# Kernel optimization log

Measured on AMD Instinct MI355X. Metric: run time of the kernel, lower is better.

## Reference

```python
import jax, jax.numpy as jnp
import numpy as np

DIST_THRESH = 150.0
ROW_EPS = 1e-6
BN_EPS = 1e-5


def setup_inputs() -> dict:
    key = jax.random.key(0)
    ks = jax.random.split(key, 6)
    B, N, T, D = 64, 64, 16, 512
    person_features = jax.random.normal(ks[0], (B, N, T, D), dtype=jnp.float32)
    # bboxes in pixel-ish units so the 150px threshold gives a mixed adjacency
    bboxes = jax.random.uniform(ks[1], (B, N, 4), dtype=jnp.float32) * 300.0
    w1 = jax.random.normal(ks[2], (D, D), dtype=jnp.float32) * (1.0 / np.sqrt(D))
    b1 = jax.random.normal(ks[3], (D,), dtype=jnp.float32) * 0.02
    w2 = jax.random.normal(ks[4], (D, D), dtype=jnp.float32) * (1.0 / np.sqrt(D))
    b2 = jax.random.normal(ks[5], (D,), dtype=jnp.float32) * 0.02
    g1 = jnp.ones((D,), jnp.float32); beta1 = jnp.zeros((D,), jnp.float32)
    g2 = jnp.ones((D,), jnp.float32); beta2 = jnp.zeros((D,), jnp.float32)
    return {"person_features": person_features, "bboxes": bboxes,
            "w1": w1, "b1": b1, "g1": g1, "beta1": beta1,
            "w2": w2, "b2": b2, "g2": g2, "beta2": beta2}


def _build_adjacency(bboxes):
    # centers: (B, N, 2) from x+w/2, y+h/2
    cx = bboxes[..., 0] + 0.5 * bboxes[..., 2]
    cy = bboxes[..., 1] + 0.5 * bboxes[..., 3]
    centers = jnp.stack([cx, cy], axis=-1)
    # pairwise distances (B, N, N), vectorized (replaces B*N*N python loop)
    diff = centers[:, :, None, :] - centers[:, None, :, :]
    dist = jnp.sqrt(jnp.sum(diff * diff, axis=-1))
    N = bboxes.shape[1]
    eye = jnp.eye(N, dtype=bboxes.dtype)
    off_diag = (eye[None] == 0.0)
    A = jnp.where((dist < DIST_THRESH) & off_diag, 1.0, 0.0) + eye[None]
    return A


def _stgcn(x, A, w, b, g, beta):
    # x: (B, N, C); A: (B, N, N)
    # torch: A_norm = A / (A.sum(dim=1 of A[i] -> axis=2) + eps)
    A_norm = A / (jnp.sum(A, axis=2, keepdims=True) + ROW_EPS)
    # x_graph = x[b].T @ A_norm[b]  -> (B, C, N)
    y = jnp.einsum('bnc,bnm->bcm', x, A_norm)
    # 1x1 conv == channel GEMM, bias added per out-channel
    y = jnp.einsum('oc,bcm->bom', w, y) + b[None, :, None]
    # BatchNorm2d in training mode: biased stats over (batch, spatial)
    mean = jnp.mean(y, axis=(0, 2), keepdims=True)
    var = jnp.mean(jnp.square(y - mean), axis=(0, 2), keepdims=True)
    y = (y - mean) / jnp.sqrt(var + BN_EPS)
    y = y * g[None, :, None] + beta[None, :, None]
    y = jax.nn.relu(y)
    return jnp.swapaxes(y, 1, 2)  # (B, N, C)


def reference(person_features, bboxes, w1, b1, g1, beta1, w2, b2, g2, beta2):
    A = _build_adjacency(bboxes)
    x = person_features[:, :, -1, :]  # (B, N, D) last frame
    h = _stgcn(x, A, w1, b1, g1, beta1)
    h = _stgcn(h, A, w2, b2, g2, beta2)
    # write enhanced features back into last timestep
    return person_features.at[:, :, -1, :].set(h)
```

## Files before the change

### kernel.cpp

```cpp
#include <hip/hip_runtime.h>
#include <hip/hip_bf16.h>


typedef __attribute__((ext_vector_type(8))) short short8;
typedef __attribute__((ext_vector_type(4))) float v4f;

#define DIST_THRESH 150.0f
#define ROW_EPS 1e-6f
#define BN_EPS 1e-5f

__device__ __forceinline__ ushort f2bf(float f) {
  union { __hip_bfloat16 h; ushort u; } cv;
  cv.h = __float2bfloat16(f);
  return cv.u;
}

__global__ __launch_bounds__(256) void k_copy_prep(const float4* __restrict__ in,
                                                   float4* __restrict__ out,
                                                   const float* __restrict__ w1,
                                                   const float* __restrict__ w2,
                                                   ushort* __restrict__ wb,
                                                   float* __restrict__ stats) {
  int blk = blockIdx.x;
  int t = threadIdx.x;
  if (blk < 8192) {
    size_t i = (size_t)blk * 256 + t;
#pragma unroll
    for (int j = 0; j < 4; ++j) {
      size_t idx = i + (size_t)j * 2097152;
      int tt = (int)((idx >> 7) & 15);
      if (tt != 15) out[idx] = in[idx];
    }
  } else {
    int idx = (blk - 8192) * 256 + t;
    float v = (idx < 262144) ? w1[idx] : w2[idx - 262144];
    wb[idx] = f2bf(v);
    if (idx < 2048) stats[idx] = 0.f;
  }
}

__global__ __launch_bounds__(256) void k_agg(const float* __restrict__ Xbase,
                                             int rowStride,
                                             const float* __restrict__ bb,
                                             const float* __restrict__ stats,
                                             const float* __restrict__ g,
                                             const float* __restrict__ beta,
                                             int applyBN,
                                             ushort* __restrict__ Z) {
  int b = blockIdx.x;
  int c0 = blockIdx.y * 128;
  int t = threadIdx.x;
  __shared__ float Xs[64][128];
  __shared__ float As[64][64];
  __shared__ float cxs[64], cys[64];
  __shared__ float scaleS[128], shiftS[128];

  if (t < 64) {
    float4 v = *(const float4*)&bb[(size_t)(b * 64 + t) * 4];
    cxs[t] = v.x + 0.5f * v.z;
    cys[t] = v.y + 0.5f * v.w;
  }
  if (applyBN && t < 32) {
    int c = t * 4;
    float4 sm = *(const float4*)&stats[c0 + c];
    float4 sq = *(const float4*)&stats[512 + c0 + c];
    float4 gg = *(const float4*)&g[c0 + c];
    float4 bt = *(const float4*)&beta[c0 + c];
    const float inv = 1.0f / 4096.0f;
    float mean, var, sc;
    mean = sm.x * inv; var = sq.x * inv - mean * mean; sc = gg.x * rsqrtf(var + BN_EPS);
    scaleS[c] = sc; shiftS[c] = bt.x - mean * sc;
    mean = sm.y * inv; var = sq.y * inv - mean * mean; sc = gg.y * rsqrtf(var + BN_EPS);
    scaleS[c + 1] = sc; shiftS[c + 1] = bt.y - mean * sc;
    mean = sm.z * inv; var = sq.z * inv - mean * mean; sc = gg.z * rsqrtf(var + BN_EPS);
    scaleS[c + 2] = sc; shiftS[c + 2] = bt.z - mean * sc;
    mean = sm.w * inv; var = sq.w * inv - mean * mean; sc = gg.w * rsqrtf(var + BN_EPS);
    scaleS[c + 3] = sc; shiftS[c + 3] = bt.w - mean * sc;
  }
  __syncthreads();

  if (t < 64) {
    float mycx = cxs[t], mycy = cys[t];
    float rs = 0.f;
    for (int m = 0; m < 64; ++m) {
      float dx = mycx - cxs[m], dy = mycy - cys[m];
      float d = sqrtf(dx * dx + dy * dy);
      float a = (m == t) ? 1.0f : ((d < DIST_THRESH) ? 1.0f : 0.0f);
      rs += a;
    }
    float inv = 1.0f / (rs + ROW_EPS);
    for (int m = 0; m < 64; ++m) {
      float dx = mycx - cxs[m], dy = mycy - cys[m];
      float d = sqrtf(dx * dx + dy * dy);
      float a = (m == t) ? 1.0f : ((d < DIST_THRESH) ? 1.0f : 0.0f);
      As[t][m] = a * inv;
    }
  }

  const float* xb = Xbase + (size_t)b * 64 * rowStride;
  for (int i = t; i < 2048; i += 256) {
    int n = i >> 5, c4 = (i & 31) << 2;
    float4 x = *(const float4*)&xb[(size_t)n * rowStride + c0 + c4];
    if (applyBN) {
      x.x = fmaxf(x.x * scaleS[c4] + shiftS[c4], 0.f);
      x.y = fmaxf(x.y * scaleS[c4 + 1] + shiftS[c4 + 1], 0.f);
      x.z = fmaxf(x.z * scaleS[c4 + 2] + shiftS[c4 + 2], 0.f);
      x.w = fmaxf(x.w * scaleS[c4 + 3] + shiftS[c4 + 3], 0.f);
    }
    *(float4*)&Xs[n][c4] = x;
  }
  __syncthreads();

  int c4 = (t & 31) << 2;
  int m0 = (t >> 5) << 3;
  float4 acc[8];
#pragma unroll
  for (int i = 0; i < 8; ++i) acc[i] = make_float4(0.f, 0.f, 0.f, 0.f);

  for (int n = 0; n < 64; ++n) {
    float4 x = *(const float4*)&Xs[n][c4];
    float4 a0 = *(const float4*)&As[n][m0];
    float4 a1 = *(const float4*)&As[n][m0 + 4];
    float as[8] = {a0.x, a0.y, a0.z, a0.w, a1.x, a1.y, a1.z, a1.w};
#pragma unroll
    for (int i = 0; i < 8; ++i) {
      acc[i].x = fmaf(as[i], x.x, acc[i].x);
      acc[i].y = fmaf(as[i], x.y, acc[i].y);
      acc[i].z = fmaf(as[i], x.z, acc[i].z);
      acc[i].w = fmaf(as[i], x.w, acc[i].w);
    }
  }

  size_t zbase = (size_t)b * 64 * 512 + c0 + c4;
#pragma unroll
  for (int i = 0; i < 8; ++i) {
    int m = m0 + i;
    ushort4 zz;
    zz.x = f2bf(acc[i].x);
    zz.y = f2bf(acc[i].y);
    zz.z = f2bf(acc[i].z);
    zz.w = f2bf(acc[i].w);
    *(ushort4*)&Z[zbase + (size_t)m * 512] = zz;
  }
}

__global__ __launch_bounds__(256) void k_gemm(const ushort* __restrict__ Z,
                                              const ushort* __restrict__ W,
                                              const float* __restrict__ bias,
                                              float* __restrict__ Y,
                                              float* __restrict__ sum,
                                              float* __restrict__ sumsq) {
  __shared__ __align__(16) ushort Zs[64 * 40];
  __shared__ __align__(16) ushort Ws[64 * 40];
  __shared__ float redS[4][64], redQ[4][64];

  int t = threadIdx.x;
  int r0 = blockIdx.x * 64;
  int o0 = blockIdx.y * 64;
  int wv = t >> 6, lane = t & 63;
  int m = lane & 15, q = lane >> 4;

  v4f acc[4];
#pragma unroll
  for (int nf = 0; nf < 4; ++nf) acc[nf] = (v4f){0.f, 0.f, 0.f, 0.f};

  int srow = t >> 2, scg = (t & 3) << 3;

  for (int ks = 0; ks < 16; ++ks) {
    int k0 = ks * 32;
    __syncthreads();
    uint4 zv = *(const uint4*)&Z[(size_t)(r0 + srow) * 512 + k0 + scg];
    uint4 wvv = *(const uint4*)&W[(size_t)(o0 + srow) * 512 + k0 + scg];
    *(uint4*)&Zs[srow * 40 + scg] = zv;
    *(uint4*)&Ws[srow * 40 + scg] = wvv;
    __syncthreads();

    short8 a = *(const short8*)&Zs[(wv * 16 + m) * 40 + q * 8];
#pragma unroll
    for (int nf = 0; nf < 4; ++nf) {
      short8 bfr = *(const short8*)&Ws[(nf * 16 + m) * 40 + q * 8];
      acc[nf] = __builtin_amdgcn_mfma_f32_16x16x32_bf16(a, bfr, acc[nf], 0, 0, 0);
    }
  }

#pragma unroll
  for (int nf = 0; nf < 4; ++nf) {
    int col = o0 + nf * 16 + m;
    float bv = bias[col];
    float s = 0.f, s2 = 0.f;
#pragma unroll
    for (int reg = 0; reg < 4; ++reg) {
      int row = r0 + wv * 16 + q * 4 + reg;
      float y = acc[nf][reg] + bv;
      Y[(size_t)row * 512 + col] = y;
      s += y;
      s2 += y * y;
    }
    s += __shfl_xor(s, 16);
    s += __shfl_xor(s, 32);
    s2 += __shfl_xor(s2, 16);
    s2 += __shfl_xor(s2, 32);
    if (q == 0) {
      redS[wv][nf * 16 + m] = s;
      redQ[wv][nf * 16 + m] = s2;
    }
  }
  __syncthreads();
  if (t < 64) {
    float s = redS[0][t] + redS[1][t] + redS[2][t] + redS[3][t];
    float s2 = redQ[0][t] + redQ[1][t] + redQ[2][t] + redQ[3][t];
    atomicAdd(&sum[o0 + t], s);
    atomicAdd(&sumsq[o0 + t], s2);
  }
}

__global__ __launch_bounds__(256) void k_norm(const float* __restrict__ Y,
                                              const float* __restrict__ sum,
                                              const float* __restrict__ sumsq,
                                              const float* __restrict__ g,
                                              const float* __restrict__ beta,
                                              float* __restrict__ out) {
  int idx = blockIdx.x * 256 + threadIdx.x;
  int o = (idx & 127) << 2;
  int r = idx >> 7;
  float4 y = *(const float4*)&Y[(size_t)r * 512 + o];
  float4 sm = *(const float4*)&sum[o];
  float4 sq = *(const float4*)&sumsq[o];
  float4 gg = *(const float4*)&g[o];
  float4 bb = *(const float4*)&beta[o];
  const float inv = 1.0f / 4096.0f;
  float4 h;
  {
    float mean = sm.x * inv, var = sq.x * inv - mean * mean;
    h.x = fmaxf(gg.x * (y.x - mean) * rsqrtf(var + BN_EPS) + bb.x, 0.f);
  }
  {
    float mean = sm.y * inv, var = sq.y * inv - mean * mean;
    h.y = fmaxf(gg.y * (y.y - mean) * rsqrtf(var + BN_EPS) + bb.y, 0.f);
  }
  {
    float mean = sm.z * inv, var = sq.z * inv - mean * mean;
    h.z = fmaxf(gg.z * (y.z - mean) * rsqrtf(var + BN_EPS) + bb.z, 0.f);
  }
  {
    float mean = sm.w * inv, var = sq.w * inv - mean * mean;
    h.w = fmaxf(gg.w * (y.w - mean) * rsqrtf(var + BN_EPS) + bb.w, 0.f);
  }
  *(float4*)&out[((size_t)r * 16 + 15) * 512 + o] = h;
}

extern "C" void kernel_launch(void* const* d_in, const int* in_sizes, int n_in,
                              void* d_out, int out_size, void* d_ws, size_t ws_size,
                              hipStream_t stream) {
  const float* pf = (const float*)d_in[0];
  const float* bboxes = (const float*)d_in[1];
  const float* w1 = (const float*)d_in[2];
  const float* b1 = (const float*)d_in[3];
  const float* g1 = (const float*)d_in[4];
  const float* be1 = (const float*)d_in[5];
  const float* w2 = (const float*)d_in[6];
  const float* b2 = (const float*)d_in[7];
  const float* g2 = (const float*)d_in[8];
  const float* be2 = (const float*)d_in[9];
  float* out = (float*)d_out;

  ushort* wb = (ushort*)d_ws;
  ushort* Zb = wb + 524288;
  float* Yb = (float*)(Zb + 2097152);
  float* stats = Yb + 2097152;
  float* sum1 = stats;
  float* sq1 = stats + 512;
  float* sum2 = stats + 1024;
  float* sq2 = stats + 1536;

  k_copy_prep<<<10240, 256, 0, stream>>>((const float4*)pf, (float4*)out, w1, w2, wb, stats);

  k_agg<<<dim3(64, 4), 256, 0, stream>>>(pf + 7680, 8192, bboxes, stats, g1, be1, 0, Zb);
  k_gemm<<<dim3(64, 8), 256, 0, stream>>>(Zb, wb, b1, Yb, sum1, sq1);

  k_agg<<<dim3(64, 4), 256, 0, stream>>>(Yb, 512, bboxes, stats, g1, be1, 1, Zb);
  k_gemm<<<dim3(64, 8), 256, 0, stream>>>(Zb, wb + 262144, b2, Yb, sum2, sq2);

  k_norm<<<2048, 256, 0, stream>>>(Yb, sum2, sq2, g2, be2, out);
}
```

Before: 318.6 us.

## Prefetch GEMM tiles into registers, parallelize adjacency, contiguous block copy

The GEMM loop now loads the next K-slice of Z and W into registers while the current slice is consumed from shared memory, so global load latency is hidden behind MFMA work. Adjacency construction is spread over all 256 threads, with partial row sums reduced in shared memory, instead of being done serially by 64 threads. The feature copy now has each block copy a contiguous 1024-float4 chunk and no longer skips the last timestep. That removes the per-element branch but copies slightly more data, which a later kernel then overwrites.

```diff
diff --git a/kernel.cpp b/kernel.cpp
--- a/kernel.cpp
+++ b/kernel.cpp
@@ -24,13 +24,15 @@
   int blk = blockIdx.x;
   int t = threadIdx.x;
   if (blk < 8192) {
-    size_t i = (size_t)blk * 256 + t;
-#pragma unroll
-    for (int j = 0; j < 4; ++j) {
-      size_t idx = i + (size_t)j * 2097152;
-      int tt = (int)((idx >> 7) & 15);
-      if (tt != 15) out[idx] = in[idx];
-    }
+    size_t base = (size_t)blk * 1024 + t;
+    float4 r0 = in[base];
+    float4 r1 = in[base + 256];
+    float4 r2 = in[base + 512];
+    float4 r3 = in[base + 768];
+    out[base] = r0;
+    out[base + 256] = r1;
+    out[base + 512] = r2;
+    out[base + 768] = r3;
   } else {
     int idx = (blk - 8192) * 256 + t;
     float v = (idx < 262144) ? w1[idx] : w2[idx - 262144];
@@ -54,6 +56,8 @@
   __shared__ float As[64][64];
   __shared__ float cxs[64], cys[64];
   __shared__ float scaleS[128], shiftS[128];
+  __shared__ float rsum[64][4];
+  __shared__ float invr[64];
 
   if (t < 64) {
     float4 v = *(const float4*)&bb[(size_t)(b * 64 + t) * 4];
@@ -79,22 +83,21 @@
   }
   __syncthreads();
 
-  if (t < 64) {
-    float mycx = cxs[t], mycy = cys[t];
-    float rs = 0.f;
-    for (int m = 0; m < 64; ++m) {
+  int an = t >> 2, aq = t & 3;
+  float av[16];
+  {
+    float mycx = cxs[an], mycy = cys[an];
+    float ps = 0.f;
+#pragma unroll
+    for (int j = 0; j < 16; ++j) {
+      int m = aq * 16 + j;
       float dx = mycx - cxs[m], dy = mycy - cys[m];
       float d = sqrtf(dx * dx + dy * dy);
-      float a = (m == t) ? 1.0f : ((d < DIST_THRESH) ? 1.0f : 0.0f);
-      rs += a;
-    }
-    float inv = 1.0f / (rs + ROW_EPS);
-    for (int m = 0; m < 64; ++m) {
-      float dx = mycx - cxs[m], dy = mycy - cys[m];
-      float d = sqrtf(dx * dx + dy * dy);
-      float a = (m == t) ? 1.0f : ((d < DIST_THRESH) ? 1.0f : 0.0f);
-      As[t][m] = a * inv;
-    }
+      float a = (m == an) ? 1.0f : ((d < DIST_THRESH) ? 1.0f : 0.0f);
+      av[j] = a;
+      ps += a;
+    }
+    rsum[an][aq] = ps;
   }
 
   const float* xb = Xbase + (size_t)b * 64 * rowStride;
@@ -111,6 +114,17 @@
   }
   __syncthreads();
 
+  if (t < 64)
+    invr[t] = 1.0f / (rsum[t][0] + rsum[t][1] + rsum[t][2] + rsum[t][3] + ROW_EPS);
+  __syncthreads();
+
+  {
+    float iv = invr[an];
+#pragma unroll
+    for (int j = 0; j < 16; ++j) As[an][aq * 16 + j] = av[j] * iv;
+  }
+  __syncthreads();
+
   int c4 = (t & 31) << 2;
   int m0 = (t >> 5) << 3;
   float4 acc[8];
@@ -165,15 +179,22 @@
   for (int nf = 0; nf < 4; ++nf) acc[nf] = (v4f){0.f, 0.f, 0.f, 0.f};
 
   int srow = t >> 2, scg = (t & 3) << 3;
+  const ushort* zp = &Z[(size_t)(r0 + srow) * 512 + scg];
+  const ushort* wp = &W[(size_t)(o0 + srow) * 512 + scg];
+
+  uint4 zv = *(const uint4*)zp;
+  uint4 wvv = *(const uint4*)wp;
 
   for (int ks = 0; ks < 16; ++ks) {
-    int k0 = ks * 32;
     __syncthreads();
-    uint4 zv = *(const uint4*)&Z[(size_t)(r0 + srow) * 512 + k0 + scg];
-    uint4 wvv = *(const uint4*)&W[(size_t)(o0 + srow) * 512 + k0 + scg];
     *(uint4*)&Zs[srow * 40 + scg] = zv;
     *(uint4*)&Ws[srow * 40 + scg] = wvv;
     __syncthreads();
+
+    if (ks < 15) {
+      zv = *(const uint4*)(zp + (ks + 1) * 32);
+      wvv = *(const uint4*)(wp + (ks + 1) * 32);
+    }
 
     short8 a = *(const short8*)&Zs[(wv * 16 + m) * 40 + q * 8];
 #pragma unroll
```

After: 296.0 us. 7.1% less time.
